# Optimization experiments

Measured on AMD Instinct MI355X. Metric: run time of the kernel, lower is better.

## Reference

```python
import jax, jax.numpy as jnp
import numpy as np

DIM = 1536
HEADS = 12
HD = DIM // HEADS  # 128
EPS = 1e-6
SINK_SIZE = 1          # frames
MAX_ATTN = 1920        # tokens (sliding window)


def setup_inputs() -> dict:
    key = jax.random.key(0)
    ks = jax.random.split(key, 10)
    B = 1
    F, H, W = 8, 16, 24
    L = F * H * W  # 3072
    s = 0.02
    inp = {
        "x": jax.random.normal(ks[0], (B, L, DIM), jnp.float32),
        "seq_lens": jnp.array([L], jnp.int32),
        "grid_sizes": jnp.array([[F, H, W]], jnp.int32),
        "freqs": jax.random.normal(ks[1], (1024, HD // 2, 2), jnp.float32),
        "wq": jax.random.normal(ks[2], (DIM, DIM), jnp.float32) * s,
        "bq": jnp.zeros((DIM,), jnp.float32),
        "wk": jax.random.normal(ks[3], (DIM, DIM), jnp.float32) * s,
        "bk": jnp.zeros((DIM,), jnp.float32),
        "wv": jax.random.normal(ks[4], (DIM, DIM), jnp.float32) * s,
        "bv": jnp.zeros((DIM,), jnp.float32),
        "wo": jax.random.normal(ks[5], (DIM, DIM), jnp.float32) * s,
        "bo": jnp.zeros((DIM,), jnp.float32),
        "nq_w": jnp.ones((DIM,), jnp.float32),
        "nk_w": jnp.ones((DIM,), jnp.float32),
    }
    return inp


def _rmsnorm(x, w):
    # WanRMSNorm: x * rsqrt(mean(x^2) + eps) * weight
    return x * jax.lax.rsqrt(jnp.mean(x * x, axis=-1, keepdims=True) + EPS) * w


def _rope(x, F, H, W, fc):
    # x: [B, L, n, d]; fc: complex [1024, d//2]
    B, L, n, d = x.shape
    c = d // 2
    c1 = c - 2 * (c // 3)  # temporal split
    c2 = c // 3
    f0, f1, f2 = fc[:, :c1], fc[:, c1:c1 + c2], fc[:, c1 + c2:]
    fr = jnp.concatenate([
        jnp.broadcast_to(f0[:F, None, None, :], (F, H, W, c1)),
        jnp.broadcast_to(f1[None, :H, None, :], (F, H, W, c2)),
        jnp.broadcast_to(f2[None, None, :W, :], (F, H, W, c2)),
    ], axis=-1).reshape(L, 1, c)  # [L, 1, c]
    xp = x.reshape(B, L, n, c, 2)
    xc = jax.lax.complex(xp[..., 0], xp[..., 1])  # [B, L, n, c]
    xr = xc * fr[None]
    return jnp.stack([jnp.real(xr), jnp.imag(xr)], axis=-1).reshape(B, L, n, d)


def reference(x, seq_lens, grid_sizes, freqs, wq, bq, wk, bk, wv, bv, wo, bo, nq_w, nk_w):
    B, L, _ = x.shape
    gs = np.asarray(grid_sizes)[0]
    F, H, W = int(gs[0]), int(gs[1]), int(gs[2])
    fs = H * W  # frame_seqlen
    sink = SINK_SIZE * fs

    q = _rmsnorm(x @ wq.T + bq, nq_w).reshape(B, L, HEADS, HD)
    k = _rmsnorm(x @ wk.T + bk, nk_w).reshape(B, L, HEADS, HD)
    v = (x @ wv.T + bv).reshape(B, L, HEADS, HD)

    fc = jax.lax.complex(freqs[..., 0], freqs[..., 1])  # [1024, HD//2]
    q = _rope(q, F, H, W, fc)
    k = _rope(k, F, H, W, fc)

    # sink + windowed frame-causal block mask (flex_attention block_mask)
    idx = jnp.arange(L)
    qf = idx // fs
    kf = idx // fs
    mask = (kf[None, :] <= qf[:, None]) & (
        (idx[None, :] < sink) | (idx[None, :] >= (qf[:, None] + 1) * fs - MAX_ATTN)
    )  # [L, L]

    scale = 1.0 / np.float32(np.sqrt(HD))
    scores = jnp.einsum('bqnd,bknd->bnqk', q, k) * scale
    scores = jnp.where(mask[None, None], scores, jnp.float32(-1e30))
    attn = jax.nn.softmax(scores, axis=-1)
    out = jnp.einsum('bnqk,bknd->bqnd', attn, v).reshape(B, L, DIM)
    return out @ wo.T + bo
```

## Files before the change

### kernel.cpp

```cpp
#include <hip/hip_runtime.h>
#include <stdint.h>

#define DIMC 1536
#define LTOK 3072
#define HEADS 12
#define HD 128
#define FS 384
#define MAXATTN 1920
#define HTOK 1152
#define NHT 1920

typedef __attribute__((ext_vector_type(4))) float f32x4;
typedef __attribute__((ext_vector_type(8))) short bf16x8;
typedef __attribute__((ext_vector_type(4))) unsigned int u32x4;

__device__ __forceinline__ unsigned short f2bf(float f) {
  union { float f; unsigned int u; } c; c.f = f;
  unsigned int u = c.u + 0x7fffu + ((c.u >> 16) & 1u);
  return (unsigned short)(u >> 16);
}
__device__ __forceinline__ float bf2f(unsigned short s) {
  union { unsigned int u; float f; } c; c.u = (unsigned int)s << 16; return c.f;
}

__device__ __forceinline__ void dma16(const void* g, void* l) {
  __builtin_amdgcn_global_load_lds(
      (const __attribute__((address_space(1))) unsigned int*)g,
      (__attribute__((address_space(3))) unsigned int*)l, 16, 0, 0);
}

__device__ __forceinline__ int vperm4(int G) {
  return (((G >> 3) & 1) << 3) | (((G >> 1) & 1) << 2) | ((G & 1) << 1) | ((G >> 2) & 1);
}

__global__ __launch_bounds__(256)
void cvt_all_k(const float* __restrict__ x, const float* __restrict__ wq,
               const float* __restrict__ wk, const float* __restrict__ wv,
               const float* __restrict__ wo,
               unsigned short* __restrict__ xb, unsigned short* __restrict__ wqb,
               unsigned short* __restrict__ wkb, unsigned short* __restrict__ wvb,
               unsigned short* __restrict__ wob)
{
  const int i = blockIdx.x * 256 + threadIdx.x;
  const int n0 = LTOK * DIMC / 4;
  const int nw = DIMC * DIMC / 4;
  const float* src; unsigned short* dst; int off;
  if (i < n0) { src = x; dst = xb; off = i; }
  else {
    int j = i - n0; int w = j / nw; off = j - w * nw;
    src = (w == 0) ? wq : (w == 1) ? wk : (w == 2) ? wv : wo;
    dst = (w == 0) ? wqb : (w == 1) ? wkb : (w == 2) ? wvb : wob;
  }
  float4 f = ((const float4*)src)[off];
  uint2 o;
  o.x = (unsigned int)f2bf(f.x) | ((unsigned int)f2bf(f.y) << 16);
  o.y = (unsigned int)f2bf(f.z) | ((unsigned int)f2bf(f.w) << 16);
  ((uint2*)dst)[off] = o;
}

__global__ __launch_bounds__(256)
void gemm_qkv(const unsigned short* __restrict__ A,
              const unsigned short* __restrict__ B0,
              const unsigned short* __restrict__ B1,
              const unsigned short* __restrict__ B2,
              const float* __restrict__ bias0,
              const float* __restrict__ bias1,
              const float* __restrict__ bias2,
              unsigned short* __restrict__ o0, unsigned short* __restrict__ o1,
              unsigned short* __restrict__ vt)
{
  const int z = blockIdx.z;
  const unsigned short* Bw = (z == 0) ? B0 : (z == 1) ? B1 : B2;
  const float* bias = (z == 0) ? bias0 : (z == 1) ? bias1 : bias2;

  __shared__ __align__(16) unsigned short lA[128 * 64];
  __shared__ __align__(16) unsigned short lB[128 * 64];

  const int tid = threadIdx.x;
  const int wave = tid >> 6;
  const int lane = tid & 63;
  const int m0 = blockIdx.y * 128;
  const int n0 = blockIdx.x * 128;
  const int wm = (wave >> 1) * 64;
  const int wn = (wave & 1) * 64;

  f32x4 acc[4][4] = {};

  const int srow = tid >> 3;
  const int scol = ((tid & 7) ^ (srow & 7)) * 8;
  const unsigned short* ga = A  + (size_t)(m0 + srow) * DIMC + scol;
  const unsigned short* gb = Bw + (size_t)(n0 + srow) * DIMC + scol;
  unsigned short* la = lA + tid * 8;
  unsigned short* lb = lB + tid * 8;

  const int fr = lane & 15;
  const int g = lane >> 4;
  const int fx = fr & 7;

  for (int k0 = 0; k0 < DIMC; k0 += 64) {
    dma16(ga + k0,                     la);
    dma16(ga + k0 + (size_t)32 * DIMC, la + 2048);
    dma16(ga + k0 + (size_t)64 * DIMC, la + 4096);
    dma16(ga + k0 + (size_t)96 * DIMC, la + 6144);
    dma16(gb + k0,                     lb);
    dma16(gb + k0 + (size_t)32 * DIMC, lb + 2048);
    dma16(gb + k0 + (size_t)64 * DIMC, lb + 4096);
    dma16(gb + k0 + (size_t)96 * DIMC, lb + 6144);
    __syncthreads();

#pragma unroll
    for (int kk = 0; kk < 2; ++kk) {
      const int cx = ((kk * 4 + g) ^ fx) * 8;
      bf16x8 af[4], bf[4];
#pragma unroll
      for (int i = 0; i < 4; ++i)
        af[i] = *(const bf16x8*)&lA[(wm + i * 16 + fr) * 64 + cx];
#pragma unroll
      for (int j = 0; j < 4; ++j)
        bf[j] = *(const bf16x8*)&lB[(wn + j * 16 + fr) * 64 + cx];
#pragma unroll
      for (int i = 0; i < 4; ++i)
#pragma unroll
        for (int j = 0; j < 4; ++j)
          acc[i][j] = __builtin_amdgcn_mfma_f32_16x16x32_bf16(af[i], bf[j], acc[i][j], 0, 0, 0);
    }
    __syncthreads();
  }

  const int col = lane & 15;
  const int rb = (lane >> 4) * 4;
  if (z < 2) {
    unsigned short* outp = z ? o1 : o0;
#pragma unroll
    for (int j = 0; j < 4; ++j) {
      const int gn = n0 + wn + j * 16 + col;
      const float bv = bias[gn];
#pragma unroll
      for (int i = 0; i < 4; ++i)
#pragma unroll
        for (int r = 0; r < 4; ++r) {
          const int gm = m0 + wm + i * 16 + rb + r;
          outp[(size_t)gm * DIMC + gn] = f2bf(acc[i][j][r] + bv);
        }
    }
  } else {
#pragma unroll
    for (int j = 0; j < 4; ++j) {
      const int gn = n0 + wn + j * 16 + col;
      const float bv = bias[gn];
#pragma unroll
      for (int i = 0; i < 4; ++i) {
        const int base = wm + i * 16 + rb;
        const int tile = base & ~63;
        const int toka = m0 + tile + vperm4((base & 63) >> 2) * 4;
        uint2 pk;
        pk.x = (unsigned int)f2bf(acc[i][j][0] + bv) |
               ((unsigned int)f2bf(acc[i][j][1] + bv) << 16);
        pk.y = (unsigned int)f2bf(acc[i][j][2] + bv) |
               ((unsigned int)f2bf(acc[i][j][3] + bv) << 16);
        *(uint2*)(vt + (size_t)gn * LTOK + toka) = pk;
      }
    }
  }
}

__global__ __launch_bounds__(256)
void gemm_wo(const unsigned short* __restrict__ A,
             const unsigned short* __restrict__ Bw,
             const float* __restrict__ bias,
             float* __restrict__ outp)
{
  __shared__ __align__(16) unsigned short lA[64 * 64];
  __shared__ __align__(16) unsigned short lB[128 * 64];

  const int tid = threadIdx.x;
  const int wave = tid >> 6;
  const int lane = tid & 63;
  const int m0 = blockIdx.y * 64;
  const int n0 = blockIdx.x * 128;
  const int wm = (wave >> 1) * 32;
  const int wn = (wave & 1) * 64;

  f32x4 acc[2][4] = {};

  const int srow = tid >> 3;
  const int scol = ((tid & 7) ^ (srow & 7)) * 8;
  const unsigned short* ga = A  + (size_t)(m0 + srow) * DIMC + scol;
  const unsigned short* gb = Bw + (size_t)(n0 + srow) * DIMC + scol;
  unsigned short* la = lA + tid * 8;
  unsigned short* lb = lB + tid * 8;

  const int fr = lane & 15;
  const int g = lane >> 4;
  const int fx = fr & 7;

  for (int k0 = 0; k0 < DIMC; k0 += 64) {
    dma16(ga + k0,                     la);
    dma16(ga + k0 + (size_t)32 * DIMC, la + 2048);
    dma16(gb + k0,                     lb);
    dma16(gb + k0 + (size_t)32 * DIMC, lb + 2048);
    dma16(gb + k0 + (size_t)64 * DIMC, lb + 4096);
    dma16(gb + k0 + (size_t)96 * DIMC, lb + 6144);
    __syncthreads();

#pragma unroll
    for (int kk = 0; kk < 2; ++kk) {
      const int cx = ((kk * 4 + g) ^ fx) * 8;
      bf16x8 af[2], bf[4];
#pragma unroll
      for (int i = 0; i < 2; ++i)
        af[i] = *(const bf16x8*)&lA[(wm + i * 16 + fr) * 64 + cx];
#pragma unroll
      for (int j = 0; j < 4; ++j)
        bf[j] = *(const bf16x8*)&lB[(wn + j * 16 + fr) * 64 + cx];
#pragma unroll
      for (int i = 0; i < 2; ++i)
#pragma unroll
        for (int j = 0; j < 4; ++j)
          acc[i][j] = __builtin_amdgcn_mfma_f32_16x16x32_bf16(af[i], bf[j], acc[i][j], 0, 0, 0);
    }
    __syncthreads();
  }

  const int col = lane & 15;
  const int rb = (lane >> 4) * 4;
#pragma unroll
  for (int j = 0; j < 4; ++j) {
    const int gn = n0 + wn + j * 16 + col;
    const float bv = bias[gn];
#pragma unroll
    for (int i = 0; i < 2; ++i)
#pragma unroll
      for (int r = 0; r < 4; ++r) {
        const int gm = m0 + wm + i * 16 + rb + r;
        outp[(size_t)gm * DIMC + gn] = acc[i][j][r] + bv;
      }
  }
}

__global__ __launch_bounds__(256)
void post_qkv_k(unsigned short* __restrict__ q, unsigned short* __restrict__ k,
                const float* __restrict__ nqw, const float* __restrict__ nkw,
                const float* __restrict__ freqs)
{
  const int bx = blockIdx.x;
  const int tid = threadIdx.x;
  const int which = bx >= LTOK;
  const int tok = bx - which * LTOK;
  unsigned short* row = (which ? k : q) + (size_t)tok * DIMC;
  const float* nw = which ? nkw : nqw;
  const float sc = which ? 1.f : (0.08838834764831845f * 1.4426950408889634f);
  const int base = tid * 6;

  float vv[6];
  float ss = 0.f;
#pragma unroll
  for (int j = 0; j < 6; ++j) {
    vv[j] = bf2f(row[base + j]);
    ss += vv[j] * vv[j];
  }
#pragma unroll
  for (int off = 1; off < 64; off <<= 1) ss += __shfl_xor(ss, off);
  __shared__ float wsum[4];
  if ((tid & 63) == 0) wsum[tid >> 6] = ss;
  __syncthreads();
  const float total = wsum[0] + wsum[1] + wsum[2] + wsum[3];
  const float rms = rsqrtf(total * (1.f / DIMC) + 1e-6f);

  const int f = tok / FS;
  const int rem = tok - f * FS;
  const int h = rem / 24;
  const int w = rem - h * 24;

#pragma unroll
  for (int pp = 0; pp < 3; ++pp) {
    const int P = (base >> 1) + pp;
    const int p = P & 63;
    const int t = (p < 22) ? f : ((p < 43) ? h : w);
    const float fre = freqs[t * 128 + p * 2];
    const float fim = freqs[t * 128 + p * 2 + 1];
    const float e = vv[2 * pp]     * rms * nw[base + 2 * pp];
    const float o = vv[2 * pp + 1] * rms * nw[base + 2 * pp + 1];
    row[base + 2 * pp]     = f2bf((e * fre - o * fim) * sc);
    row[base + 2 * pp + 1] = f2bf((e * fim + o * fre) * sc);
  }
}

#define KBUF (64 * 128)
#define VBUF (128 * 64)
__global__ __launch_bounds__(256, 2)
void attn_flash(const unsigned short* __restrict__ q,
                const unsigned short* __restrict__ k,
                const unsigned short* __restrict__ vt,
                unsigned short* __restrict__ ab,
                float* __restrict__ Opart,
                float* __restrict__ mlbuf)
{
  const int bid = blockIdx.x;
  int qb, head, chunk, nchunks;
  if (bid < 360) { const int hb = bid >> 1; qb = 23 - hb / 12; head = hb % 12; chunk = bid & 1; nchunks = 2; }
  else           { const int lb = bid - 360; qb = 8 - lb / 12; head = lb % 12; chunk = 0; nchunks = 1; }

  const int q0 = qb * 128;
  const int qf = qb / 3;
  const int kend = (qf + 1) * FS;
  const int s2 = kend - MAXATTN;
  const bool two = (s2 > FS);
  const int nt1 = (two ? FS : kend) >> 6;
  const int nt  = nt1 + (two ? (MAXATTN >> 6) : 0);
  const int half = nt / nchunks;
  const int tstart = chunk * half, tend = tstart + half;

  const int tid = threadIdx.x;
  const int wave = tid >> 6, lane = tid & 63;
  const int col = lane & 15;
  const int g = lane >> 4;
  const int g4 = g * 4;

  __shared__ __align__(16) unsigned short Kl[2 * KBUF];
  __shared__ __align__(16) unsigned short Vtl[2 * VBUF];

  bf16x8 qfA[4], qfB[4];
  {
    const unsigned short* qr0 = q + (size_t)(q0 + wave * 32 + col) * DIMC + head * HD;
#pragma unroll
    for (int kk = 0; kk < 4; ++kk) {
      qfA[kk] = *(const bf16x8*)(qr0 + kk * 32 + g * 8);
      qfB[kk] = *(const bf16x8*)(qr0 + (size_t)16 * DIMC + kk * 32 + g * 8);
    }
  }

  f32x4 o0[8] = {}, o1[8] = {};
  float m0 = -3.0e38f, l0 = 0.f, m1 = -3.0e38f, l1 = 0.f;

  const int krow = tid >> 4;
  const int kc8  = ((tid & 15) ^ krow) * 8;
  const unsigned short* kg = k + (size_t)krow * DIMC + head * HD + kc8;
  const int vrow = tid >> 3;
  const int vc8  = ((tid & 7) ^ (vrow & 7)) * 8;
  const unsigned short* vg = vt + ((size_t)head * HD + vrow) * LTOK + vc8;
  unsigned short* kl = Kl + tid * 8;
  unsigned short* vl = Vtl + tid * 8;

  {
    const int kb = (tstart < nt1) ? tstart * 64 : s2 + (tstart - nt1) * 64;
    const unsigned short* kp = kg + (size_t)kb * DIMC;
    dma16(kp,                     kl);
    dma16(kp + (size_t)16 * DIMC, kl + 16 * 128);
    dma16(kp + (size_t)32 * DIMC, kl + 32 * 128);
    dma16(kp + (size_t)48 * DIMC, kl + 48 * 128);
    const unsigned short* vp = vg + kb;
    dma16(vp,                     vl);
    dma16(vp + (size_t)32 * LTOK, vl + 32 * 64);
    dma16(vp + (size_t)64 * LTOK, vl + 64 * 64);
    dma16(vp + (size_t)96 * LTOK, vl + 96 * 64);
  }

  for (int t = tstart; t < tend; ++t) {
    const int kcur = ((t - tstart) & 1) * KBUF;
    const int vcur = ((t - tstart) & 1) * VBUF;
    __syncthreads();

    if (t + 1 < tend) {
      const int kb = (t + 1 < nt1) ? (t + 1) * 64 : s2 + (t + 1 - nt1) * 64;
      const int knxt = KBUF - kcur, vnxt = VBUF - vcur;
      const unsigned short* kp = kg + (size_t)kb * DIMC;
      dma16(kp,                     kl + knxt);
      dma16(kp + (size_t)16 * DIMC, kl + knxt + 16 * 128);
      dma16(kp + (size_t)32 * DIMC, kl + knxt + 32 * 128);
      dma16(kp + (size_t)48 * DIMC, kl + knxt + 48 * 128);
      const unsigned short* vp = vg + kb;
      dma16(vp,                     vl + vnxt);
      dma16(vp + (size_t)32 * LTOK, vl + vnxt + 32 * 64);
      dma16(vp + (size_t)64 * LTOK, vl + vnxt + 64 * 64);
      dma16(vp + (size_t)96 * LTOK, vl + vnxt + 96 * 64);
    }

    f32x4 sA[4] = {}, sB[4] = {};
#pragma unroll
    for (int kt = 0; kt < 4; ++kt) {
      const unsigned short* kr = &Kl[kcur + (kt * 16 + col) * 128];
#pragma unroll
      for (int kk = 0; kk < 4; ++kk) {
        bf16x8 kfr = *(const bf16x8*)(kr + ((kk * 4 + g) ^ col) * 8);
        sA[kt] = __builtin_amdgcn_mfma_f32_16x16x32_bf16(kfr, qfA[kk], sA[kt], 0, 0, 0);
        sB[kt] = __builtin_amdgcn_mfma_f32_16x16x32_bf16(kfr, qfB[kk], sB[kt], 0, 0, 0);
      }
    }

    unsigned int A0, A1, A2, A3, A4, A5, A6, A7;
    float alA;
    {
      float mx = sA[0][0];
#pragma unroll
      for (int kt = 0; kt < 4; ++kt)
#pragma unroll
        for (int r = 0; r < 4; ++r) mx = fmaxf(mx, sA[kt][r]);
      mx = fmaxf(mx, __shfl_xor(mx, 16));
      mx = fmaxf(mx, __shfl_xor(mx, 32));
      const float mn = fmaxf(m0, mx);
      alA = exp2f(m0 - mn);
      m0 = mn;
      float rs = 0.f;
#define PKA(KT, PA, PB)                                        \
      {                                                        \
        const unsigned short p0 = f2bf(exp2f(sA[KT][0] - mn)); \
        const unsigned short p1 = f2bf(exp2f(sA[KT][1] - mn)); \
        const unsigned short p2 = f2bf(exp2f(sA[KT][2] - mn)); \
        const unsigned short p3 = f2bf(exp2f(sA[KT][3] - mn)); \
        rs += bf2f(p0) + bf2f(p1) + bf2f(p2) + bf2f(p3);       \
        PA = (unsigned int)p0 | ((unsigned int)p1 << 16);      \
        PB = (unsigned int)p2 | ((unsigned int)p3 << 16);      \
      }
      PKA(0, A0, A1) PKA(1, A2, A3) PKA(2, A4, A5) PKA(3, A6, A7)
#undef PKA
      rs += __shfl_xor(rs, 16);
      rs += __shfl_xor(rs, 32);
      l0 = l0 * alA + rs;
    }
    unsigned int B0, B1, B2, B3, B4, B5, B6, B7;
    float alB;
    {
      float mx = sB[0][0];
#pragma unroll
      for (int kt = 0; kt < 4; ++kt)
#pragma unroll
        for (int r = 0; r < 4; ++r) mx = fmaxf(mx, sB[kt][r]);
      mx = fmaxf(mx, __shfl_xor(mx, 16));
      mx = fmaxf(mx, __shfl_xor(mx, 32));
      const float mn = fmaxf(m1, mx);
      alB = exp2f(m1 - mn);
      m1 = mn;
      float rs = 0.f;
#define PKB(KT, PA, PB)                                        \
      {                                                        \
        const unsigned short p0 = f2bf(exp2f(sB[KT][0] - mn)); \
        const unsigned short p1 = f2bf(exp2f(sB[KT][1] - mn)); \
        const unsigned short p2 = f2bf(exp2f(sB[KT][2] - mn)); \
        const unsigned short p3 = f2bf(exp2f(sB[KT][3] - mn)); \
        rs += bf2f(p0) + bf2f(p1) + bf2f(p2) + bf2f(p3);       \
        PA = (unsigned int)p0 | ((unsigned int)p1 << 16);      \
        PB = (unsigned int)p2 | ((unsigned int)p3 << 16);      \
      }
      PKB(0, B0, B1) PKB(1, B2, B3) PKB(2, B4, B5) PKB(3, B6, B7)
#undef PKB
      rs += __shfl_xor(rs, 16);
      rs += __shfl_xor(rs, 32);
      l1 = l1 * alB + rs;
    }

#pragma unroll
    for (int dt = 0; dt < 8; ++dt) { o0[dt] *= alA; o1[dt] *= alB; }

    u32x4 tA0, tA1, tB0, tB1;
    tA0[0] = A0; tA0[1] = A1; tA0[2] = A2; tA0[3] = A3;
    tA1[0] = A4; tA1[1] = A5; tA1[2] = A6; tA1[3] = A7;
    tB0[0] = B0; tB0[1] = B1; tB0[2] = B2; tB0[3] = B3;
    tB1[0] = B4; tB1[1] = B5; tB1[2] = B6; tB1[3] = B7;
    const bf16x8 pfA0 = __builtin_bit_cast(bf16x8, tA0);
    const bf16x8 pfA1 = __builtin_bit_cast(bf16x8, tA1);
    const bf16x8 pfB0 = __builtin_bit_cast(bf16x8, tB0);
    const bf16x8 pfB1 = __builtin_bit_cast(bf16x8, tB1);

    const int vx0 = (g ^ (col & 7)) * 8;
    const int vx1 = ((4 + g) ^ (col & 7)) * 8;
#pragma unroll
    for (int dt = 0; dt < 8; ++dt) {
      const unsigned short* vr = &Vtl[vcur + (dt * 16 + col) * 64];
      bf16x8 vf0 = *(const bf16x8*)(vr + vx0);
      o0[dt] = __builtin_amdgcn_mfma_f32_16x16x32_bf16(vf0, pfA0, o0[dt], 0, 0, 0);
      o1[dt] = __builtin_amdgcn_mfma_f32_16x16x32_bf16(vf0, pfB0, o1[dt], 0, 0, 0);
      bf16x8 vf1 = *(const bf16x8*)(vr + vx1);
      o0[dt] = __builtin_amdgcn_mfma_f32_16x16x32_bf16(vf1, pfA1, o0[dt], 0, 0, 0);
      o1[dt] = __builtin_amdgcn_mfma_f32_16x16x32_bf16(vf1, pfB1, o1[dt], 0, 0, 0);
    }
  }

  const int qrow0 = q0 + wave * 32 + col;
  if (nchunks == 1) {
    const float i0 = 1.f / l0, i1 = 1.f / l1;
    unsigned short* or0 = ab + (size_t)qrow0 * DIMC + head * HD;
    unsigned short* or1 = or0 + (size_t)16 * DIMC;
#pragma unroll
    for (int dt = 0; dt < 8; ++dt) {
      uint2 pk;
      pk.x = (unsigned int)f2bf(o0[dt][0] * i0) | ((unsigned int)f2bf(o0[dt][1] * i0) << 16);
      pk.y = (unsigned int)f2bf(o0[dt][2] * i0) | ((unsigned int)f2bf(o0[dt][3] * i0) << 16);
      *(uint2*)(or0 + dt * 16 + g4) = pk;
      pk.x = (unsigned int)f2bf(o1[dt][0] * i1) | ((unsigned int)f2bf(o1[dt][1] * i1) << 16);
      pk.y = (unsigned int)f2bf(o1[dt][2] * i1) | ((unsigned int)f2bf(o1[dt][3] * i1) << 16);
      *(uint2*)(or1 + dt * 16 + g4) = pk;
    }
  } else {
    const int tokp0 = qrow0 - HTOK;
    float* ob0 = Opart + ((size_t)(chunk * NHT + tokp0) * HEADS + head) * HD;
    float* ob1 = Opart + ((size_t)(chunk * NHT + tokp0 + 16) * HEADS + head) * HD;
#pragma unroll
    for (int dt = 0; dt < 8; ++dt) {
      *(f32x4*)(ob0 + dt * 16 + g4) = o0[dt];
      *(f32x4*)(ob1 + dt * 16 + g4) = o1[dt];
    }
    if (lane < 16) {
      float* mlp0 = mlbuf + 2 * ((size_t)(chunk * NHT + tokp0) * HEADS + head);
      float* mlp1 = mlbuf + 2 * ((size_t)(chunk * NHT + tokp0 + 16) * HEADS + head);
      mlp0[0] = m0; mlp0[1] = l0;
      mlp1[0] = m1; mlp1[1] = l1;
    }
  }
}

__global__ __launch_bounds__(384)
void merge_k(const float* __restrict__ Opart, const float* __restrict__ mlbuf,
             unsigned short* __restrict__ ab)
{
  const int tokp = blockIdx.x;
  const int tid = threadIdx.x;
  const int e = tid * 4;
  const int head = e >> 7;
  const size_t r0 = (size_t)tokp * DIMC + e;
  float4 o0 = *(const float4*)(Opart + r0);
  float4 o1 = *(const float4*)(Opart + (size_t)NHT * DIMC + r0);
  const float* ml0 = mlbuf + 2 * ((size_t)tokp * HEADS + head);
  const float* ml1 = mlbuf + 2 * ((size_t)(NHT + tokp) * HEADS + head);
  const float m0 = ml0[0], l0 = ml0[1], m1 = ml1[0], l1 = ml1[1];
  const float mm = fmaxf(m0, m1);
  const float a0 = exp2f(m0 - mm), a1 = exp2f(m1 - mm);
  const float inv = 1.f / (l0 * a0 + l1 * a1);
  uint2 pk;
  pk.x = (unsigned int)f2bf((o0.x * a0 + o1.x * a1) * inv) |
         ((unsigned int)f2bf((o0.y * a0 + o1.y * a1) * inv) << 16);
  pk.y = (unsigned int)f2bf((o0.z * a0 + o1.z * a1) * inv) |
         ((unsigned int)f2bf((o0.w * a0 + o1.w * a1) * inv) << 16);
  *(uint2*)(ab + (size_t)(HTOK + tokp) * DIMC + e) = pk;
}

extern "C" void kernel_launch(void* const* d_in, const int* in_sizes, int n_in,
                              void* d_out, int out_size, void* d_ws, size_t ws_size,
                              hipStream_t stream)
{
  (void)in_sizes; (void)n_in; (void)out_size; (void)ws_size;
  const float* x     = (const float*)d_in[0];
  const float* freqs = (const float*)d_in[3];
  const float* wq    = (const float*)d_in[4];
  const float* bq    = (const float*)d_in[5];
  const float* wk    = (const float*)d_in[6];
  const float* bk    = (const float*)d_in[7];
  const float* wv    = (const float*)d_in[8];
  const float* bv    = (const float*)d_in[9];
  const float* wo    = (const float*)d_in[10];
  const float* bo    = (const float*)d_in[11];
  const float* nqw   = (const float*)d_in[12];
  const float* nkw   = (const float*)d_in[13];

  char* ws = (char*)d_ws;
  size_t off = 0;
  auto take = [&](size_t bytes) -> void* {
    void* p = ws + off; off += (bytes + 255) & ~(size_t)255; return p;
  };
  unsigned short* wob = (unsigned short*)take((size_t)DIMC * DIMC * 2);
  unsigned short* qb  = (unsigned short*)take((size_t)LTOK * DIMC * 2);
  unsigned short* kb  = (unsigned short*)take((size_t)LTOK * DIMC * 2);
  unsigned short* vb  = (unsigned short*)take((size_t)LTOK * DIMC * 2);
  unsigned short* ab  = (unsigned short*)take((size_t)LTOK * DIMC * 2);
  unsigned short* vtb = (unsigned short*)take((size_t)LTOK * DIMC * 2);
  unsigned short* xb  = (unsigned short*)take((size_t)LTOK * DIMC * 2);
  unsigned short* wqb = (unsigned short*)take((size_t)DIMC * DIMC * 2);
  unsigned short* wkb = (unsigned short*)take((size_t)DIMC * DIMC * 2);
  unsigned short* wvb = (unsigned short*)take((size_t)DIMC * DIMC * 2);
  float* mlb = (float*)take((size_t)2 * NHT * HEADS * 2 * sizeof(float));
  float* Opart = (float*)xb;
  (void)vb;

  cvt_all_k<<<dim3(13824), dim3(256), 0, stream>>>(x, wq, wk, wv, wo,
                                                   xb, wqb, wkb, wvb, wob);

  gemm_qkv<<<dim3(DIMC / 128, LTOK / 128, 3), dim3(256), 0, stream>>>(
      xb, wqb, wkb, wvb, bq, bk, bv, qb, kb, vtb);

  post_qkv_k<<<dim3(2 * LTOK), dim3(256), 0, stream>>>(qb, kb, nqw, nkw, freqs);

  attn_flash<<<dim3(468), dim3(256), 0, stream>>>(qb, kb, vtb, ab, Opart, mlb);
  merge_k<<<dim3(NHT), dim3(384), 0, stream>>>(Opart, mlb, ab);

  gemm_wo<<<dim3(DIMC / 128, LTOK / 64), dim3(256), 0, stream>>>(
      ab, wob, bo, (float*)d_out);
}
```

Baseline: 285.0 us.

## Split attention KV range into more chunks and single-buffer LDS for occupancy

Attention work is repartitioned: late query blocks are split four ways, middle blocks two ways, and only the earliest blocks run unsplit, giving 900 blocks instead of 468. The K/V LDS double buffer is dropped to single buffering with an extra barrier, and launch bounds are raised to 4 blocks per SM so that occupancy hides latency instead of software prefetch. Partial outputs for the four-way split are stored in bf16 and combined by a new merge kernel, with a second merge kernel for the two-way blocks. This trades extra merge traffic, an additional launch and some precision loss in the partials for better load balance and occupancy.

```diff
diff --git a/kernel.cpp b/kernel.cpp
--- a/kernel.cpp
+++ b/kernel.cpp
@@ -9,6 +9,8 @@
 #define MAXATTN 1920
 #define HTOK 1152
 #define NHT 1920
+#define MTOK 384
+#define NMT 768
 
 typedef __attribute__((ext_vector_type(4))) float f32x4;
 typedef __attribute__((ext_vector_type(8))) short bf16x8;
@@ -286,20 +288,19 @@
   }
 }
 
-#define KBUF (64 * 128)
-#define VBUF (128 * 64)
-__global__ __launch_bounds__(256, 2)
+__global__ __launch_bounds__(256, 4)
 void attn_flash(const unsigned short* __restrict__ q,
                 const unsigned short* __restrict__ k,
                 const unsigned short* __restrict__ vt,
                 unsigned short* __restrict__ ab,
-                float* __restrict__ Opart,
-                float* __restrict__ mlbuf)
+                unsigned short* __restrict__ OpH, float* __restrict__ mlH,
+                float* __restrict__ OpM, float* __restrict__ mlM)
 {
   const int bid = blockIdx.x;
   int qb, head, chunk, nchunks;
-  if (bid < 360) { const int hb = bid >> 1; qb = 23 - hb / 12; head = hb % 12; chunk = bid & 1; nchunks = 2; }
-  else           { const int lb = bid - 360; qb = 8 - lb / 12; head = lb % 12; chunk = 0; nchunks = 1; }
+  if (bid < 720)      { const int qh = bid >> 2; chunk = bid & 3; nchunks = 4; qb = 23 - qh / 12; head = qh % 12; }
+  else if (bid < 864) { const int mb = bid - 720; const int qh = mb >> 1; chunk = mb & 1; nchunks = 2; qb = 8 - qh / 12; head = qh % 12; }
+  else                { const int lb = bid - 864; qb = 2 - lb / 12; head = lb % 12; chunk = 0; nchunks = 1; }
 
   const int q0 = qb * 128;
   const int qf = qb / 3;
@@ -308,8 +309,8 @@
   const bool two = (s2 > FS);
   const int nt1 = (two ? FS : kend) >> 6;
   const int nt  = nt1 + (two ? (MAXATTN >> 6) : 0);
-  const int half = nt / nchunks;
-  const int tstart = chunk * half, tend = tstart + half;
+  const int tstart = chunk * nt / nchunks;
+  const int tend = (chunk + 1) * nt / nchunks;
 
   const int tid = threadIdx.x;
   const int wave = tid >> 6, lane = tid & 63;
@@ -317,8 +318,8 @@
   const int g = lane >> 4;
   const int g4 = g * 4;
 
-  __shared__ __align__(16) unsigned short Kl[2 * KBUF];
-  __shared__ __align__(16) unsigned short Vtl[2 * VBUF];
+  __shared__ __align__(16) unsigned short Kl[64 * 128];
+  __shared__ __align__(16) unsigned short Vtl[128 * 64];
 
   bf16x8 qfA[4], qfB[4];
   {
@@ -342,8 +343,8 @@
   unsigned short* kl = Kl + tid * 8;
   unsigned short* vl = Vtl + tid * 8;
 
-  {
-    const int kb = (tstart < nt1) ? tstart * 64 : s2 + (tstart - nt1) * 64;
+  for (int t = tstart; t < tend; ++t) {
+    const int kb = (t < nt1) ? t * 64 : s2 + (t - nt1) * 64;
     const unsigned short* kp = kg + (size_t)kb * DIMC;
     dma16(kp,                     kl);
     dma16(kp + (size_t)16 * DIMC, kl + 16 * 128);
@@ -354,32 +355,12 @@
     dma16(vp + (size_t)32 * LTOK, vl + 32 * 64);
     dma16(vp + (size_t)64 * LTOK, vl + 64 * 64);
     dma16(vp + (size_t)96 * LTOK, vl + 96 * 64);
-  }
-
-  for (int t = tstart; t < tend; ++t) {
-    const int kcur = ((t - tstart) & 1) * KBUF;
-    const int vcur = ((t - tstart) & 1) * VBUF;
     __syncthreads();
 
-    if (t + 1 < tend) {
-      const int kb = (t + 1 < nt1) ? (t + 1) * 64 : s2 + (t + 1 - nt1) * 64;
-      const int knxt = KBUF - kcur, vnxt = VBUF - vcur;
-      const unsigned short* kp = kg + (size_t)kb * DIMC;
-      dma16(kp,                     kl + knxt);
-      dma16(kp + (size_t)16 * DIMC, kl + knxt + 16 * 128);
-      dma16(kp + (size_t)32 * DIMC, kl + knxt + 32 * 128);
-      dma16(kp + (size_t)48 * DIMC, kl + knxt + 48 * 128);
-      const unsigned short* vp = vg + kb;
-      dma16(vp,                     vl + vnxt);
-      dma16(vp + (size_t)32 * LTOK, vl + vnxt + 32 * 64);
-      dma16(vp + (size_t)64 * LTOK, vl + vnxt + 64 * 64);
-      dma16(vp + (size_t)96 * LTOK, vl + vnxt + 96 * 64);
-    }
-
     f32x4 sA[4] = {}, sB[4] = {};
 #pragma unroll
     for (int kt = 0; kt < 4; ++kt) {
-      const unsigned short* kr = &Kl[kcur + (kt * 16 + col) * 128];
+      const unsigned short* kr = &Kl[(kt * 16 + col) * 128];
 #pragma unroll
       for (int kk = 0; kk < 4; ++kk) {
         bf16x8 kfr = *(const bf16x8*)(kr + ((kk * 4 + g) ^ col) * 8);
@@ -466,7 +447,7 @@
     const int vx1 = ((4 + g) ^ (col & 7)) * 8;
 #pragma unroll
     for (int dt = 0; dt < 8; ++dt) {
-      const unsigned short* vr = &Vtl[vcur + (dt * 16 + col) * 64];
+      const unsigned short* vr = &Vtl[(dt * 16 + col) * 64];
       bf16x8 vf0 = *(const bf16x8*)(vr + vx0);
       o0[dt] = __builtin_amdgcn_mfma_f32_16x16x32_bf16(vf0, pfA0, o0[dt], 0, 0, 0);
       o1[dt] = __builtin_amdgcn_mfma_f32_16x16x32_bf16(vf0, pfB0, o1[dt], 0, 0, 0);
@@ -474,6 +455,7 @@
       o0[dt] = __builtin_amdgcn_mfma_f32_16x16x32_bf16(vf1, pfA1, o0[dt], 0, 0, 0);
       o1[dt] = __builtin_amdgcn_mfma_f32_16x16x32_bf16(vf1, pfB1, o1[dt], 0, 0, 0);
     }
+    __syncthreads();
   }
 
   const int qrow0 = q0 + wave * 32 + col;
@@ -491,37 +473,100 @@
       pk.y = (unsigned int)f2bf(o1[dt][2] * i1) | ((unsigned int)f2bf(o1[dt][3] * i1) << 16);
       *(uint2*)(or1 + dt * 16 + g4) = pk;
     }
-  } else {
-    const int tokp0 = qrow0 - HTOK;
-    float* ob0 = Opart + ((size_t)(chunk * NHT + tokp0) * HEADS + head) * HD;
-    float* ob1 = Opart + ((size_t)(chunk * NHT + tokp0 + 16) * HEADS + head) * HD;
+  } else if (nchunks == 2) {
+    const int tokm0 = qrow0 - MTOK;
+    float* ob0 = OpM + ((size_t)(chunk * NMT + tokm0) * HEADS + head) * HD;
+    float* ob1 = OpM + ((size_t)(chunk * NMT + tokm0 + 16) * HEADS + head) * HD;
 #pragma unroll
     for (int dt = 0; dt < 8; ++dt) {
       *(f32x4*)(ob0 + dt * 16 + g4) = o0[dt];
       *(f32x4*)(ob1 + dt * 16 + g4) = o1[dt];
     }
     if (lane < 16) {
-      float* mlp0 = mlbuf + 2 * ((size_t)(chunk * NHT + tokp0) * HEADS + head);
-      float* mlp1 = mlbuf + 2 * ((size_t)(chunk * NHT + tokp0 + 16) * HEADS + head);
-      mlp0[0] = m0; mlp0[1] = l0;
-      mlp1[0] = m1; mlp1[1] = l1;
+      float* p0 = mlM + 2 * ((size_t)(chunk * NMT + tokm0) * HEADS + head);
+      float* p1 = mlM + 2 * ((size_t)(chunk * NMT + tokm0 + 16) * HEADS + head);
+      p0[0] = m0; p0[1] = l0;
+      p1[0] = m1; p1[1] = l1;
+    }
+  } else {
+    const int tokp0 = qrow0 - HTOK;
+    unsigned short* ob0 = OpH + ((size_t)(chunk * NHT + tokp0) * HEADS + head) * HD;
+    unsigned short* ob1 = OpH + ((size_t)(chunk * NHT + tokp0 + 16) * HEADS + head) * HD;
+#pragma unroll
+    for (int dt = 0; dt < 8; ++dt) {
+      uint2 pk;
+      pk.x = (unsigned int)f2bf(o0[dt][0]) | ((unsigned int)f2bf(o0[dt][1]) << 16);
+      pk.y = (unsigned int)f2bf(o0[dt][2]) | ((unsigned int)f2bf(o0[dt][3]) << 16);
+      *(uint2*)(ob0 + dt * 16 + g4) = pk;
+      pk.x = (unsigned int)f2bf(o1[dt][0]) | ((unsigned int)f2bf(o1[dt][1]) << 16);
+      pk.y = (unsigned int)f2bf(o1[dt][2]) | ((unsigned int)f2bf(o1[dt][3]) << 16);
+      *(uint2*)(ob1 + dt * 16 + g4) = pk;
+    }
+    if (lane < 16) {
+      float* p0 = mlH + 2 * ((size_t)(chunk * NHT + tokp0) * HEADS + head);
+      float* p1 = mlH + 2 * ((size_t)(chunk * NHT + tokp0 + 16) * HEADS + head);
+      p0[0] = m0; p0[1] = l0;
+      p1[0] = m1; p1[1] = l1;
     }
   }
 }
 
 __global__ __launch_bounds__(384)
-void merge_k(const float* __restrict__ Opart, const float* __restrict__ mlbuf,
+void merge_h(const unsigned short* __restrict__ OpH, const float* __restrict__ mlH,
              unsigned short* __restrict__ ab)
 {
   const int tokp = blockIdx.x;
   const int tid = threadIdx.x;
   const int e = tid * 4;
   const int head = e >> 7;
-  const size_t r0 = (size_t)tokp * DIMC + e;
-  float4 o0 = *(const float4*)(Opart + r0);
-  float4 o1 = *(const float4*)(Opart + (size_t)NHT * DIMC + r0);
-  const float* ml0 = mlbuf + 2 * ((size_t)tokp * HEADS + head);
-  const float* ml1 = mlbuf + 2 * ((size_t)(NHT + tokp) * HEADS + head);
+  const int d = e & 127;
+
+  float mc0, mc1, mc2, mc3, lc0, lc1, lc2, lc3;
+  {
+    const float* p0 = mlH + 2 * ((size_t)(0 * NHT + tokp) * HEADS + head);
+    const float* p1 = mlH + 2 * ((size_t)(1 * NHT + tokp) * HEADS + head);
+    const float* p2 = mlH + 2 * ((size_t)(2 * NHT + tokp) * HEADS + head);
+    const float* p3 = mlH + 2 * ((size_t)(3 * NHT + tokp) * HEADS + head);
+    mc0 = p0[0]; lc0 = p0[1]; mc1 = p1[0]; lc1 = p1[1];
+    mc2 = p2[0]; lc2 = p2[1]; mc3 = p3[0]; lc3 = p3[1];
+  }
+  const float mm = fmaxf(fmaxf(mc0, mc1), fmaxf(mc2, mc3));
+  const float a0 = exp2f(mc0 - mm), a1 = exp2f(mc1 - mm);
+  const float a2 = exp2f(mc2 - mm), a3 = exp2f(mc3 - mm);
+  const float inv = 1.f / (lc0 * a0 + lc1 * a1 + lc2 * a2 + lc3 * a3);
+
+  float acc0 = 0.f, acc1 = 0.f, acc2 = 0.f, acc3 = 0.f;
+#define ACCC(C, AC)                                                        \
+  {                                                                        \
+    uint2 v = *(const uint2*)(OpH + ((size_t)(C * NHT + tokp) * HEADS + head) * HD + d); \
+    acc0 += AC * bf2f((unsigned short)(v.x & 0xffff));                     \
+    acc1 += AC * bf2f((unsigned short)(v.x >> 16));                        \
+    acc2 += AC * bf2f((unsigned short)(v.y & 0xffff));                     \
+    acc3 += AC * bf2f((unsigned short)(v.y >> 16));                        \
+  }
+  ACCC(0, a0) ACCC(1, a1) ACCC(2, a2) ACCC(3, a3)
+#undef ACCC
+  uint2 pk;
+  pk.x = (unsigned int)f2bf(acc0 * inv) | ((unsigned int)f2bf(acc1 * inv) << 16);
+  pk.y = (unsigned int)f2bf(acc2 * inv) | ((unsigned int)f2bf(acc3 * inv) << 16);
+  *(uint2*)(ab + (size_t)(HTOK + tokp) * DIMC + e) = pk;
+}
+
+__global__ __launch_bounds__(384)
+void merge_m(const float* __restrict__ OpM, const float* __restrict__ mlM,
+             unsigned short* __restrict__ ab)
+{
+  const int tokm = blockIdx.x;
+  const int tid = threadIdx.x;
+  const int e = tid * 4;
+  const int head = e >> 7;
+  const int d = e & 127;
+  const size_t r0 = ((size_t)(0 * NMT + tokm) * HEADS + head) * HD + d;
+  const size_t r1 = ((size_t)(1 * NMT + tokm) * HEADS + head) * HD + d;
+  float4 o0 = *(const float4*)(OpM + r0);
+  float4 o1 = *(const float4*)(OpM + r1);
+  const float* ml0 = mlM + 2 * ((size_t)(0 * NMT + tokm) * HEADS + head);
+  const float* ml1 = mlM + 2 * ((size_t)(1 * NMT + tokm) * HEADS + head);
   const float m0 = ml0[0], l0 = ml0[1], m1 = ml1[0], l1 = ml1[1];
   const float mm = fmaxf(m0, m1);
   const float a0 = exp2f(m0 - mm), a1 = exp2f(m1 - mm);
@@ -531,7 +576,7 @@
          ((unsigned int)f2bf((o0.y * a0 + o1.y * a1) * inv) << 16);
   pk.y = (unsigned int)f2bf((o0.z * a0 + o1.z * a1) * inv) |
          ((unsigned int)f2bf((o0.w * a0 + o1.w * a1) * inv) << 16);
-  *(uint2*)(ab + (size_t)(HTOK + tokp) * DIMC + e) = pk;
+  *(uint2*)(ab + (size_t)(MTOK + tokm) * DIMC + e) = pk;
 }
 
 extern "C" void kernel_launch(void* const* d_in, const int* in_sizes, int n_in,
@@ -567,9 +612,10 @@
   unsigned short* wqb = (unsigned short*)take((size_t)DIMC * DIMC * 2);
   unsigned short* wkb = (unsigned short*)take((size_t)DIMC * DIMC * 2);
   unsigned short* wvb = (unsigned short*)take((size_t)DIMC * DIMC * 2);
-  float* mlb = (float*)take((size_t)2 * NHT * HEADS * 2 * sizeof(float));
-  float* Opart = (float*)xb;
-  (void)vb;
+  float* mlH = (float*)take((size_t)4 * NHT * HEADS * 2 * sizeof(float));
+  float* mlM = (float*)take((size_t)2 * NMT * HEADS * 2 * sizeof(float));
+  unsigned short* OpH = xb;
+  float* OpM = (float*)vb;
 
   cvt_all_k<<<dim3(13824), dim3(256), 0, stream>>>(x, wq, wk, wv, wo,
                                                    xb, wqb, wkb, wvb, wob);
@@ -579,8 +625,10 @@
 
   post_qkv_k<<<dim3(2 * LTOK), dim3(256), 0, stream>>>(qb, kb, nqw, nkw, freqs);
 
-  attn_flash<<<dim3(468), dim3(256), 0, stream>>>(qb, kb, vtb, ab, Opart, mlb);
-  merge_k<<<dim3(NHT), dim3(384), 0, stream>>>(Opart, mlb, ab);
+  attn_flash<<<dim3(900), dim3(256), 0, stream>>>(qb, kb, vtb, ab,
+                                                  OpH, mlH, OpM, mlM);
+  merge_h<<<dim3(NHT), dim3(384), 0, stream>>>(OpH, mlH, ab);
+  merge_m<<<dim3(NMT), dim3(384), 0, stream>>>(OpM, mlM, ab);
 
   gemm_wo<<<dim3(DIMC / 128, LTOK / 64), dim3(256), 0, stream>>>(
       ab, wob, bo, (float*)d_out);
```

Result: slower. 368.7 us (+29.4%).
